# Kernel tuning notes

Hardware: AMD Instinct MI355X
Metric: run time of the kernel (lower is better)

Reference implementation:

```python
import jax, jax.numpy as jnp
import numpy as np

NEG = -1e30  # log-space 'zero'
BLANK = 0


def setup_inputs() -> dict:
    key = jax.random.key(0)
    T, B, V, L = 1000, 32, 2048, 64
    k1, k2 = jax.random.split(key)
    acts = jax.random.normal(k1, (T, B, V), dtype=jnp.float32)
    # concatenated labels, one sequence of length L per example, blank=0 excluded
    labels = jax.random.randint(k2, (B * L,), 1, V, dtype=jnp.int32)
    act_lens = jnp.full((B,), T, dtype=jnp.int32)
    label_lens = jnp.full((B,), L, dtype=jnp.int32)
    return {"acts": acts, "labels": labels, "act_lens": act_lens, "label_lens": label_lens}


def _ctc_total_cost(acts, labels, act_lens, label_lens):
    # acts: (T, B, V) raw activations; warp-ctc applies softmax internally (blank=0).
    T, B, V = acts.shape
    L = labels.shape[0] // B  # uniform label length (sum(label_lens) == len(labels))
    S = 2 * L + 1
    labels2d = labels.reshape(B, L)
    # extended label sequence: blank, l1, blank, l2, ..., blank  -> (B, S)
    ext = jnp.zeros((B, S), dtype=jnp.int32).at[:, 1::2].set(labels2d)
    # transitions from s-2 allowed only for non-blank differing from ext[s-2]
    ext_m2 = jnp.concatenate([jnp.full((B, 2), -1, dtype=jnp.int32), ext[:, :-2]], axis=1)
    allow2 = (ext != BLANK) & (ext != ext_m2)  # (B, S)

    logp = jax.nn.log_softmax(acts, axis=-1)  # (T, B, V)
    # gather log-probs of extended labels: (T, B, S)
    lp_ext = jnp.take_along_axis(logp, jnp.broadcast_to(ext[None], (T, B, S)), axis=2)

    # alpha init at t=0: only s=0 (blank) and s=1 (first label)
    alpha0 = jnp.full((B, S), NEG, dtype=acts.dtype)
    alpha0 = alpha0.at[:, 0].set(lp_ext[0, :, 0]).at[:, 1].set(lp_ext[0, :, 1])

    def step(alpha, xs):
        t, lp_t = xs  # lp_t: (B, S)
        a1 = jnp.concatenate([jnp.full((B, 1), NEG, alpha.dtype), alpha[:, :-1]], axis=1)
        a2 = jnp.concatenate([jnp.full((B, 2), NEG, alpha.dtype), alpha[:, :-2]], axis=1)
        a2 = jnp.where(allow2, a2, NEG)
        new = jnp.logaddexp(jnp.logaddexp(alpha, a1), a2) + lp_t
        # freeze alpha for sequences that have already ended
        new = jnp.where((t < act_lens)[:, None], new, alpha)
        return new, None

    alphaT, _ = jax.lax.scan(step, alpha0, (jnp.arange(1, T), lp_ext[1:]))

    # terminal states: last blank (s=2*label_len) and last label (s=2*label_len-1)
    s_last = (2 * label_lens).astype(jnp.int32)  # (B,)
    a_end1 = jnp.take_along_axis(alphaT, s_last[:, None], axis=1)[:, 0]
    a_end2 = jnp.take_along_axis(alphaT, (s_last - 1)[:, None], axis=1)[:, 0]
    loss_b = -jnp.logaddexp(a_end1, a_end2)  # (B,)
    # size_average=False, length_average=False -> plain sum, returned as shape (1,)
    return jnp.sum(loss_b)[None]


def reference(acts, labels, act_lens, label_lens):
    return _ctc_total_cost(acts, labels, act_lens, label_lens)
```

## Files before the change

kernel.cpp:

```cpp
#include <hip/hip_runtime.h>
#include <stdint.h>

#define LOG2E  1.4426950408889634f
#define LN2    0.6931471805599453f

typedef float v4f __attribute__((ext_vector_type(4)));

__device__ __forceinline__ float dpp_shr1_z(float x) {
  int r = __builtin_amdgcn_update_dpp(0, __float_as_int(x), 0x138, 0xf, 0xf, true);
  return __int_as_float(r);
}

template <int CTRL>
__device__ __forceinline__ float dpp_max(float v) {
  int r = __builtin_amdgcn_update_dpp(0, __float_as_int(v), CTRL, 0xf, 0xf, true);
  return fmaxf(v, __int_as_float(r));
}

__device__ __forceinline__ float wave_max_uniform(float v) {
  v = dpp_max<0x111>(v);
  v = dpp_max<0x112>(v);
  v = dpp_max<0x114>(v);
  v = dpp_max<0x118>(v);
  v = dpp_max<0x142>(v);
  v = dpp_max<0x143>(v);
  int gm = __builtin_amdgcn_readlane(__float_as_int(v), 63);
  return __int_as_float(gm);
}

__global__ __launch_bounds__(256) void k_prob_gather(
    const float* __restrict__ acts, const int* __restrict__ labels,
    float* __restrict__ lp, int T, int Tp, int B, int V, int L) {
  const int lane = threadIdx.x & 63;
  const uint32_t r = blockIdx.x * 4u + (threadIdx.x >> 6);
  if (r >= (uint32_t)(T * B)) return;
  const uint32_t b = r / (uint32_t)T;
  const uint32_t t = r % (uint32_t)T;
  const float* __restrict__ row = acts + ((size_t)t * (size_t)B + b) * (size_t)V;

  float mx, l2s;
  if (V == 2048) {
    const float4* row4 = (const float4*)row;
    float vals[32];
    mx = -3.0e38f;
#pragma unroll
    for (int q = 0; q < 8; ++q) {
      float4 v = row4[lane + (q << 6)];
      vals[q*4+0] = v.x; vals[q*4+1] = v.y; vals[q*4+2] = v.z; vals[q*4+3] = v.w;
      mx = fmaxf(mx, fmaxf(fmaxf(v.x, v.y), fmaxf(v.z, v.w)));
    }
#pragma unroll
    for (int off = 32; off >= 1; off >>= 1) mx = fmaxf(mx, __shfl_xor(mx, off, 64));
    float s = 0.0f;
#pragma unroll
    for (int k = 0; k < 32; ++k) s += exp2f((vals[k] - mx) * LOG2E);
#pragma unroll
    for (int off = 32; off >= 1; off >>= 1) s += __shfl_xor(s, off, 64);
    l2s = log2f(s);
  } else {
    float m = -3.0e38f, s = 0.0f;
    for (int i = lane; i < V; i += 64) {
      float x = row[i];
      float m2 = fmaxf(m, x);
      s = s * exp2f((m - m2) * LOG2E) + exp2f((x - m2) * LOG2E);
      m = m2;
    }
#pragma unroll
    for (int off = 32; off >= 1; off >>= 1) {
      float mo = __shfl_xor(m, off, 64), so = __shfl_xor(s, off, 64);
      float m2 = fmaxf(m, mo);
      s = s * exp2f((m - m2) * LOG2E) + so * exp2f((mo - m2) * LOG2E);
      m = m2;
    }
    mx = m;
    l2s = log2f(s);
  }

  float* __restrict__ out = lp + (size_t)b * (size_t)(L + 1) * (size_t)Tp;
  if (lane < L) {
    int lab = labels[b * (uint32_t)L + lane];
    out[(size_t)(1 + lane) * Tp + t] = exp2f((row[lab] - mx) * LOG2E - l2s);
  }
  if (lane == 0) out[t] = exp2f((row[0] - mx) * LOG2E - l2s);
}

__global__ __launch_bounds__(64, 4) void k_ctc_fwd(
    const float* __restrict__ lp, const int* __restrict__ labels,
    const int* __restrict__ act_lens, const int* __restrict__ label_lens,
    float* __restrict__ loss, int T, int Tp, int B, int L) {
  const int b = blockIdx.x;
  const int lane = threadIdx.x;
  const int Tact = __builtin_amdgcn_readfirstlane(min(act_lens[b], T));
  const int ll   = __builtin_amdgcn_readfirstlane(min(label_lens[b], L));

  const float* __restrict__ chb = lp + (size_t)b * (size_t)(L + 1) * (size_t)Tp;
  const int lclamp = (lane < L) ? lane : (L - 1);
  const float* __restrict__ chl = chb + (size_t)(1 + lclamp) * (size_t)Tp;

  int lab_i = (lane < L) ? labels[(size_t)b * L + lane] : 0;
  int lab_p = (lane >= 1 && lane - 1 < L) ? labels[(size_t)b * L + lane - 1] : -1;
  const bool allow2 = (lane >= 1) && (lab_i != 0) && (lab_i != lab_p);

  __shared__ float S[64][17];
  __shared__ float A_[132];

  v4f r0, r1, r2, r3;
  int acc_e = 0;

#define LOADR(tt) { const float* p_ = chl + (tt);                            \
    asm volatile("global_load_dwordx4 %0, %4, off\n\t"                       \
                 "global_load_dwordx4 %1, %4, off offset:16\n\t"             \
                 "global_load_dwordx4 %2, %4, off offset:32\n\t"             \
                 "global_load_dwordx4 %3, %4, off offset:48"                 \
                 : "=&v"(r0), "=&v"(r1), "=&v"(r2), "=&v"(r3) : "v"(p_)); }

#define WAITR asm volatile("s_waitcnt vmcnt(0)"                              \
                 : "+v"(r0), "+v"(r1), "+v"(r2), "+v"(r3));

#define WRITES { S[lane][0]=r0.x;  S[lane][1]=r0.y;  S[lane][2]=r0.z;  S[lane][3]=r0.w;  \
                 S[lane][4]=r1.x;  S[lane][5]=r1.y;  S[lane][6]=r1.z;  S[lane][7]=r1.w;  \
                 S[lane][8]=r2.x;  S[lane][9]=r2.y;  S[lane][10]=r2.z; S[lane][11]=r2.w; \
                 S[lane][12]=r3.x; S[lane][13]=r3.y; S[lane][14]=r3.z; S[lane][15]=r3.w; }

#define ST(PB, PL) { float pa = dpp_shr1_z(s1);                              \
    float c2 = allow2 ? pa : 0.0f;                                           \
    float n0 = (s0 + pa) * (PB);                                             \
    float n1 = ((s0 + c2) + s1) * (PL);                                      \
    float n2 = (s2 + s1) * (PB);                                             \
    s0 = n0; s1 = n1; s2 = n2; }

#define RESC { float gm = wave_max_uniform(fmaxf(fmaxf(s0, s1), s2));        \
    int e = ((__float_as_int(gm) >> 23) & 0xff) - 127;                       \
    acc_e += e;                                                              \
    float sc = __int_as_float((127 - e) << 23);                              \
    s0 *= sc; s1 *= sc; s2 *= sc; }

#define STEPK(k, cb)  { float lpl = S[lane][k]; float lpb = (cb)[k]; ST(lpb, lpl) }
#define STEPG(k, cb, tt) { if ((tt) >= 1 && (tt) < Tact) STEPK(k, cb) }

#define WIN16(cb) { STEPK(0,cb)  STEPK(1,cb)  STEPK(2,cb)  STEPK(3,cb)  RESC \
                    STEPK(4,cb)  STEPK(5,cb)  STEPK(6,cb)  STEPK(7,cb)  RESC \
                    STEPK(8,cb)  STEPK(9,cb)  STEPK(10,cb) STEPK(11,cb) RESC \
                    STEPK(12,cb) STEPK(13,cb) STEPK(14,cb) STEPK(15,cb) RESC }

#define WIN16G(cb, tb) { STEPG(0,cb,(tb)+0)  STEPG(1,cb,(tb)+1)  STEPG(2,cb,(tb)+2)   \
                         STEPG(3,cb,(tb)+3)  RESC                                     \
                         STEPG(4,cb,(tb)+4)  STEPG(5,cb,(tb)+5)  STEPG(6,cb,(tb)+6)   \
                         STEPG(7,cb,(tb)+7)  RESC                                     \
                         STEPG(8,cb,(tb)+8)  STEPG(9,cb,(tb)+9)  STEPG(10,cb,(tb)+10) \
                         STEPG(11,cb,(tb)+11) RESC                                    \
                         STEPG(12,cb,(tb)+12) STEPG(13,cb,(tb)+13) STEPG(14,cb,(tb)+14) \
                         STEPG(15,cb,(tb)+15) RESC }

  LOADR(0)
  WAITR
  WRITES
  LOADR(16)

  float blk0 = chb[0];
  float lbl0 = S[lane][0];
  float s0 = (lane == 0) ? blk0 : 0.0f;
  float s1 = (lane == 0) ? lbl0 : 0.0f;
  float s2 = 0.0f;

  { const float* cb = chb; WIN16G(cb, 0) }

  int t0 = 16;
  while (t0 + 16 <= Tact) {
    WAITR
    WRITES
    { int tn = t0 + 16; if (tn > Tp - 16) tn = Tp - 16; LOADR(tn) }
    const float* cb = chb + t0;
    WIN16(cb)
    t0 += 16;
  }

  if (t0 < Tact) {
    WAITR
    WRITES
    const float* cb = chb + t0;
    WIN16G(cb, t0)
  }

#undef LOADR
#undef WAITR
#undef WRITES
#undef ST
#undef RESC
#undef STEPK
#undef STEPG
#undef WIN16
#undef WIN16G

  A_[2 * lane] = s0;
  A_[2 * lane + 1] = s1;
  if (lane == 63) A_[128] = s2;
  __syncthreads();
  if (lane == 0) {
    int sl = 2 * ll;
    float a1 = A_[sl];
    float a2 = (sl >= 1) ? A_[sl - 1] : 0.0f;
    loss[b] = -(logf(a1 + a2) + (float)acc_e * LN2);
  }
}

__global__ __launch_bounds__(64) void k_sum(const float* __restrict__ loss,
                                            float* __restrict__ out, int B) {
  int lane = threadIdx.x;
  float s = 0.0f;
  for (int i = lane; i < B; i += 64) s += loss[i];
#pragma unroll
  for (int off = 32; off >= 1; off >>= 1) s += __shfl_xor(s, off, 64);
  if (lane == 0) out[0] = s;
}

extern "C" void kernel_launch(void* const* d_in, const int* in_sizes, int n_in,
                              void* d_out, int out_size, void* d_ws, size_t ws_size,
                              hipStream_t stream) {
  const float* acts       = (const float*)d_in[0];
  const int*   labels     = (const int*)d_in[1];
  const int*   act_lens   = (const int*)d_in[2];
  const int*   label_lens = (const int*)d_in[3];

  const int B = in_sizes[2];
  const int L = in_sizes[1] / B;
  const int T = 1000;
  const int V = (int)((long long)in_sizes[0] / ((long long)T * (long long)B));
  const int Tp = (T + 31) & ~31;

  float* lp    = (float*)d_ws;
  float* lossb = lp + (size_t)B * (size_t)(L + 1) * (size_t)Tp;

  k_prob_gather<<<dim3((T * B + 3) / 4), dim3(256), 0, stream>>>(
      acts, labels, lp, T, Tp, B, V, L);
  k_ctc_fwd<<<dim3(B), dim3(64), 0, stream>>>(lp, labels, act_lens, label_lens,
                                              lossb, T, Tp, B, L);
  k_sum<<<dim3(1), dim3(64), 0, stream>>>(lossb, (float*)d_out, B);
}
```

Measured before the change: 137.5 us.

## Defer CTC rescaling by one window and prefetch blank probabilities into registers

```diff
diff --git a/kernel.cpp b/kernel.cpp
--- a/kernel.cpp
+++ b/kernel.cpp
@@ -3,6 +3,7 @@
 
 #define LOG2E  1.4426950408889634f
 #define LN2    0.6931471805599453f
+#define BIAS_E 32
 
 typedef float v4f __attribute__((ext_vector_type(4)));
 
@@ -84,7 +85,7 @@
   if (lane == 0) out[t] = exp2f((row[0] - mx) * LOG2E - l2s);
 }
 
-__global__ __launch_bounds__(64, 4) void k_ctc_fwd(
+__global__ __launch_bounds__(64, 1) void k_ctc_fwd(
     const float* __restrict__ lp, const int* __restrict__ labels,
     const int* __restrict__ act_lens, const int* __restrict__ label_lens,
     float* __restrict__ loss, int T, int Tp, int B, int L) {
@@ -105,7 +106,14 @@
   __shared__ float A_[132];
 
   v4f r0, r1, r2, r3;
+  float4 qb0, qb1, qb2, qb3;
+  float4 nb0, nb1, nb2, nb3;
   int acc_e = 0;
+  int pend_e = 0;
+  float pend_sc = 1.0f;
+
+  asm volatile("s_waitcnt vmcnt(0) lgkmcnt(0)" ::: "memory");
+  __builtin_amdgcn_sched_barrier(0);
 
 #define LOADR(tt) { const float* p_ = chl + (tt);                            \
     asm volatile("global_load_dwordx4 %0, %4, off\n\t"                       \
@@ -122,75 +130,88 @@
                  S[lane][8]=r2.x;  S[lane][9]=r2.y;  S[lane][10]=r2.z; S[lane][11]=r2.w; \
                  S[lane][12]=r3.x; S[lane][13]=r3.y; S[lane][14]=r3.z; S[lane][15]=r3.w; }
 
+#define LOADB(D, tt) { int tc = (tt); if (tc > Tp - 16) tc = Tp - 16;        \
+    const float4* pb4 = (const float4*)(chb + tc);                           \
+    D##0 = pb4[0]; D##1 = pb4[1]; D##2 = pb4[2]; D##3 = pb4[3]; }
+
 #define ST(PB, PL) { float pa = dpp_shr1_z(s1);                              \
     float c2 = allow2 ? pa : 0.0f;                                           \
     float n0 = (s0 + pa) * (PB);                                             \
-    float n1 = ((s0 + c2) + s1) * (PL);                                      \
+    float n1 = ((s0 + s1) + c2) * (PL);                                      \
     float n2 = (s2 + s1) * (PB);                                             \
     s0 = n0; s1 = n1; s2 = n2; }
 
-#define RESC { float gm = wave_max_uniform(fmaxf(fmaxf(s0, s1), s2));        \
-    int e = ((__float_as_int(gm) >> 23) & 0xff) - 127;                       \
-    acc_e += e;                                                              \
-    float sc = __int_as_float((127 - e) << 23);                              \
-    s0 *= sc; s1 *= sc; s2 *= sc; }
-
-#define STEPK(k, cb)  { float lpl = S[lane][k]; float lpb = (cb)[k]; ST(lpb, lpl) }
-#define STEPG(k, cb, tt) { if ((tt) >= 1 && (tt) < Tact) STEPK(k, cb) }
-
-#define WIN16(cb) { STEPK(0,cb)  STEPK(1,cb)  STEPK(2,cb)  STEPK(3,cb)  RESC \
-                    STEPK(4,cb)  STEPK(5,cb)  STEPK(6,cb)  STEPK(7,cb)  RESC \
-                    STEPK(8,cb)  STEPK(9,cb)  STEPK(10,cb) STEPK(11,cb) RESC \
-                    STEPK(12,cb) STEPK(13,cb) STEPK(14,cb) STEPK(15,cb) RESC }
-
-#define WIN16G(cb, tb) { STEPG(0,cb,(tb)+0)  STEPG(1,cb,(tb)+1)  STEPG(2,cb,(tb)+2)   \
-                         STEPG(3,cb,(tb)+3)  RESC                                     \
-                         STEPG(4,cb,(tb)+4)  STEPG(5,cb,(tb)+5)  STEPG(6,cb,(tb)+6)   \
-                         STEPG(7,cb,(tb)+7)  RESC                                     \
-                         STEPG(8,cb,(tb)+8)  STEPG(9,cb,(tb)+9)  STEPG(10,cb,(tb)+10) \
-                         STEPG(11,cb,(tb)+11) RESC                                    \
-                         STEPG(12,cb,(tb)+12) STEPG(13,cb,(tb)+13) STEPG(14,cb,(tb)+14) \
-                         STEPG(15,cb,(tb)+15) RESC }
+#define RESC { s0 *= pend_sc; s1 *= pend_sc; s2 *= pend_sc; acc_e += pend_e; \
+    float gm = wave_max_uniform(fmaxf(fmaxf(s0, s1), s2));                   \
+    int e = ((__float_as_int(gm) >> 23) & 0xff) - 127 - BIAS_E;              \
+    if (e < -126) e = -126;                                                  \
+    pend_e = e;                                                              \
+    pend_sc = __int_as_float((127 - e) << 23); }
+
+#define STG(PB, PL, tt) { if ((tt) >= 1 && (tt) < Tact) ST(PB, PL) }
+
+#define WIN16 {                                                              \
+    ST(qb0.x, S[lane][0])  ST(qb0.y, S[lane][1])                             \
+    ST(qb0.z, S[lane][2])  ST(qb0.w, S[lane][3])  RESC                       \
+    ST(qb1.x, S[lane][4])  ST(qb1.y, S[lane][5])                             \
+    ST(qb1.z, S[lane][6])  ST(qb1.w, S[lane][7])  RESC                       \
+    ST(qb2.x, S[lane][8])  ST(qb2.y, S[lane][9])                             \
+    ST(qb2.z, S[lane][10]) ST(qb2.w, S[lane][11]) RESC                       \
+    ST(qb3.x, S[lane][12]) ST(qb3.y, S[lane][13])                            \
+    ST(qb3.z, S[lane][14]) ST(qb3.w, S[lane][15]) RESC }
+
+#define WIN16G(tb) {                                                         \
+    STG(qb0.x, S[lane][0],  (tb)+0)  STG(qb0.y, S[lane][1],  (tb)+1)         \
+    STG(qb0.z, S[lane][2],  (tb)+2)  STG(qb0.w, S[lane][3],  (tb)+3)  RESC   \
+    STG(qb1.x, S[lane][4],  (tb)+4)  STG(qb1.y, S[lane][5],  (tb)+5)         \
+    STG(qb1.z, S[lane][6],  (tb)+6)  STG(qb1.w, S[lane][7],  (tb)+7)  RESC   \
+    STG(qb2.x, S[lane][8],  (tb)+8)  STG(qb2.y, S[lane][9],  (tb)+9)         \
+    STG(qb2.z, S[lane][10], (tb)+10) STG(qb2.w, S[lane][11], (tb)+11) RESC   \
+    STG(qb3.x, S[lane][12], (tb)+12) STG(qb3.y, S[lane][13], (tb)+13)        \
+    STG(qb3.z, S[lane][14], (tb)+14) STG(qb3.w, S[lane][15], (tb)+15) RESC }
+
+#define SWAPB { qb0 = nb0; qb1 = nb1; qb2 = nb2; qb3 = nb3; }
 
   LOADR(0)
+  LOADB(qb, 0)
+  LOADB(nb, 16)
   WAITR
   WRITES
   LOADR(16)
 
-  float blk0 = chb[0];
-  float lbl0 = S[lane][0];
-  float s0 = (lane == 0) ? blk0 : 0.0f;
-  float s1 = (lane == 0) ? lbl0 : 0.0f;
+  float s0 = (lane == 0) ? qb0.x : 0.0f;
+  float s1 = (lane == 0) ? S[lane][0] : 0.0f;
   float s2 = 0.0f;
 
-  { const float* cb = chb; WIN16G(cb, 0) }
-
+  WIN16G(0)
+  SWAPB LOADB(nb, 32)
   int t0 = 16;
+
   while (t0 + 16 <= Tact) {
     WAITR
     WRITES
-    { int tn = t0 + 16; if (tn > Tp - 16) tn = Tp - 16; LOADR(tn) }
-    const float* cb = chb + t0;
-    WIN16(cb)
+    LOADR(t0 + 16)
+    WIN16
+    SWAPB LOADB(nb, t0 + 32)
     t0 += 16;
   }
 
   if (t0 < Tact) {
     WAITR
     WRITES
-    const float* cb = chb + t0;
-    WIN16G(cb, t0)
+    WIN16G(t0)
   }
 
 #undef LOADR
 #undef WAITR
 #undef WRITES
+#undef LOADB
 #undef ST
 #undef RESC
-#undef STEPK
-#undef STEPG
+#undef STG
 #undef WIN16
 #undef WIN16G
+#undef SWAPB
 
   A_[2 * lane] = s0;
   A_[2 * lane + 1] = s1;
```

After: 144.2 us. 1.05x slower.
